# Performance work log

Hardware: AMD Instinct MI355X
Metric: run time of the kernel (lower is better)

## Reference

```python
import jax, jax.numpy as jnp
import numpy as np

B, T, D = 4, 2048, 256   # batch, temporal_scale, input_dim
H = 8                    # num_heads (hard-coded in module)
DH = D // H              # head dim
DFF = 512                # dim_feedforward (hard-coded)
WIN = 9                  # window_size
EPS = 1e-5               # LayerNorm eps


def _window_mask(t, h, w):
    # True = masked (disallowed). Each row j allows columns clip(j - w//2 + k, 0, t-1), k in [0, w).
    rows = jnp.arange(t)[:, None]                                   # [t,1]
    cols = jnp.clip(rows - w // 2 + jnp.arange(w)[None, :], 0, t - 1)  # [t,w]
    allowed = jnp.zeros((t, t), dtype=bool).at[rows, cols].set(True)
    # local_len == num_heads == 8: every head gets the same window mask
    return jnp.broadcast_to(~allowed, (h, t, t))                    # [H,T,T]


def setup_inputs() -> dict:
    key = jax.random.key(0)
    ks = jax.random.split(key, 6)
    s = 0.05
    return {
        "features": jax.random.normal(ks[0], (B, T, D), jnp.float32),
        "w_qkv": jax.random.normal(ks[1], (3 * D, D), jnp.float32) * s,
        "b_qkv": jnp.zeros((3 * D,), jnp.float32),
        "w_out": jax.random.normal(ks[2], (D, D), jnp.float32) * s,
        "b_out": jnp.zeros((D,), jnp.float32),
        "w1": jax.random.normal(ks[3], (DFF, D), jnp.float32) * s,
        "b1": jnp.zeros((DFF,), jnp.float32),
        "w2": jax.random.normal(ks[4], (D, DFF), jnp.float32) * s,
        "b2": jnp.zeros((D,), jnp.float32),
        "g1": jnp.ones((D,), jnp.float32),
        "be1": jnp.zeros((D,), jnp.float32),
        "g2": jnp.ones((D,), jnp.float32),
        "be2": jnp.zeros((D,), jnp.float32),
        "mask": _window_mask(T, H, WIN),
    }


def _layernorm(x, g, b):
    mu = jnp.mean(x, axis=-1, keepdims=True)
    var = jnp.var(x, axis=-1, keepdims=True)
    return (x - mu) * jax.lax.rsqrt(var + EPS) * g + b


def reference(features, w_qkv, b_qkv, w_out, b_out, w1, b1, w2, b2,
              g1, be1, g2, be2, mask):
    b, t, d = features.shape
    # --- windowed multi-head self-attention (dropout = eval-mode identity) ---
    qkv = features @ w_qkv.T + b_qkv                         # [b,t,3d]
    q, k, v = jnp.split(qkv, 3, axis=-1)
    split_heads = lambda x: x.reshape(b, t, H, DH).transpose(0, 2, 1, 3)  # [b,H,t,dh]
    q, k, v = split_heads(q), split_heads(k), split_heads(v)
    scores = jnp.einsum('bhqd,bhkd->bhqk', q, k) / jnp.sqrt(jnp.float32(DH))
    scores = jnp.where(mask[None], -jnp.inf, scores)         # mask True = disallowed
    attn = jax.nn.softmax(scores, axis=-1)                   # [b,H,t,t]
    o = jnp.einsum('bhqk,bhkd->bhqd', attn, v)
    o = o.transpose(0, 2, 1, 3).reshape(b, t, d)
    o = o @ w_out.T + b_out
    # --- residual + norm1 ---
    x = _layernorm(features + o, g1, be1)
    # --- FFN (relu) + residual + norm2 ---
    ff = jax.nn.relu(x @ w1.T + b1) @ w2.T + b2
    return _layernorm(x + ff, g2, be2)
```

## Files before the change

kernel.cpp:

```cpp
#include <hip/hip_runtime.h>
#include <math.h>

#define T_LEN 2048
#define LN_EPS 1e-5f
#define M_ROWS 8192

using u16x8  = __attribute__((ext_vector_type(8))) unsigned short;
using bf16x8 = __attribute__((ext_vector_type(8))) short;
using f32x4  = __attribute__((ext_vector_type(4))) float;

__device__ __forceinline__ unsigned short f2bf(float f) {
    unsigned int u = __float_as_uint(f);
    u += 0x7FFFu + ((u >> 16) & 1u);
    return (unsigned short)(u >> 16);
}
__device__ __forceinline__ float bf2f(unsigned short u) {
    return __uint_as_float(((unsigned int)u) << 16);
}
__device__ __forceinline__ u16x8 pack8(float4 a, float4 c) {
    u16x8 p;
    p[0] = f2bf(a.x); p[1] = f2bf(a.y); p[2] = f2bf(a.z); p[3] = f2bf(a.w);
    p[4] = f2bf(c.x); p[5] = f2bf(c.y); p[6] = f2bf(c.z); p[7] = f2bf(c.w);
    return p;
}
__device__ __forceinline__ void gload16(const void* g, void* l) {
    __builtin_amdgcn_global_load_lds(
        (const __attribute__((address_space(1))) unsigned int*)g,
        (__attribute__((address_space(3))) unsigned int*)l, 16, 0, 0);
}

__global__ __launch_bounds__(512) void qkv_gemm_f32(
    const float* __restrict__ A, const float* __restrict__ W,
    const float* __restrict__ bias,
    const float* __restrict__ wo, const float* __restrict__ w1,
    const float* __restrict__ w2,
    unsigned short* __restrict__ C, unsigned short* __restrict__ wconv)
{
    __shared__ char sm[2][40960];

    const int tid = threadIdx.x, lane = tid & 63, wid = tid >> 6;
    const int wr = wid >> 2, wcl = wid & 3;
    const int m0 = blockIdx.x * 128, n0 = blockIdx.y * 192;

    {
        const int bid = blockIdx.y * 64 + blockIdx.x;
        const int g = bid * 512 + tid;
        if (g < 40960) {
            const int e = g * 8;
            const float* src; int off;
            if (e < 65536)       { src = wo; off = 0; }
            else if (e < 196608) { src = w1; off = 65536; }
            else                 { src = w2; off = 196608; }
            const float4 a = *(const float4*)(src + (e - off));
            const float4 c = *(const float4*)(src + (e - off) + 4);
            *(u16x8*)(wconv + e) = pack8(a, c);
        }
    }

    float4 ld[5][2];
    auto LOADR = [&](int k0) {
        #pragma unroll
        for (int j = 0; j < 5; ++j) {
            const int i = j * 512 + tid;
            const float* src;
            if (i < 1024) {
                const int row = i >> 3, k8 = i & 7;
                src = A + (size_t)(m0 + row) * 256 + k0 + k8 * 8;
            } else {
                const int ii = i - 1024;
                const int row = ii >> 3, k8 = ii & 7;
                src = W + (size_t)(n0 + row) * 256 + k0 + k8 * 8;
            }
            ld[j][0] = *(const float4*)src;
            ld[j][1] = *(const float4*)(src + 4);
        }
    };
    auto CWRITE = [&](char* buf) {
        #pragma unroll
        for (int j = 0; j < 5; ++j) {
            const int i = j * 512 + tid;
            const u16x8 p = pack8(ld[j][0], ld[j][1]);
            if (i < 1024) {
                const int row = i >> 3, k8 = i & 7;
                *(u16x8*)(buf + ((row * 128 + k8 * 16) ^ ((row & 7) << 4))) = p;
            } else {
                const int ii = i - 1024;
                const int row = ii >> 3, k8 = ii & 7;
                *(u16x8*)(buf + 16384 + ((row * 128 + k8 * 16) ^ ((row & 7) << 4))) = p;
            }
        }
    };

    f32x4 acc[4][3];
    #pragma unroll
    for (int m = 0; m < 4; ++m)
        #pragma unroll
        for (int n = 0; n < 3; ++n) acc[m][n] = (f32x4)(0.f);

    LOADR(0);
    CWRITE(sm[0]);
    __syncthreads();

    #pragma unroll
    for (int k = 0; k < 4; ++k) {
        if (k < 3) LOADR((k + 1) * 64);
        char* As = sm[k & 1];
        char* Bs = sm[k & 1] + 16384;
        #pragma unroll
        for (int ks = 0; ks < 2; ++ks) {
            bf16x8 af[4], bfr[3];
            #pragma unroll
            for (int m = 0; m < 4; ++m) {
                const int row = wr * 64 + m * 16 + (lane & 15);
                const int off = (row * 128 + ks * 64 + (lane >> 4) * 16) ^ ((row & 7) << 4);
                af[m] = *(const bf16x8*)(As + off);
            }
            #pragma unroll
            for (int n = 0; n < 3; ++n) {
                const int row = wcl * 48 + n * 16 + (lane & 15);
                const int off = (row * 128 + ks * 64 + (lane >> 4) * 16) ^ ((row & 7) << 4);
                bfr[n] = *(const bf16x8*)(Bs + off);
            }
            #pragma unroll
            for (int m = 0; m < 4; ++m)
                #pragma unroll
                for (int n = 0; n < 3; ++n)
                    acc[m][n] = __builtin_amdgcn_mfma_f32_16x16x32_bf16(
                        af[m], bfr[n], acc[m][n], 0, 0, 0);
        }
        if (k < 3) CWRITE(sm[(k + 1) & 1]);
        __syncthreads();
    }

    #pragma unroll
    for (int n = 0; n < 3; ++n) {
        const int c = n0 + wcl * 48 + n * 16 + (lane & 15);
        const float bv = bias[c];
        #pragma unroll
        for (int m = 0; m < 4; ++m) {
            const int rbase = m0 + wr * 64 + m * 16 + ((lane >> 4) << 2);
            #pragma unroll
            for (int j = 0; j < 4; ++j)
                C[(size_t)(rbase + j) * 768 + c] = f2bf(acc[m][n][j] + bv);
        }
    }
}

__global__ __launch_bounds__(512) void tail_fused_db(
    const unsigned short* __restrict__ qkv, const unsigned short* __restrict__ Wo,
    const unsigned short* __restrict__ W1, const unsigned short* __restrict__ W2,
    const float* __restrict__ resf, const float* __restrict__ b_out,
    const float* __restrict__ g1, const float* __restrict__ be1,
    const float* __restrict__ b1, const float* __restrict__ b2,
    const float* __restrict__ g2, const float* __restrict__ be2,
    float* __restrict__ out)
{
    __shared__ __align__(16) char sm[116736];
    char* smA = sm;
    char* st[2] = { sm + 16384, sm + 49152 };
    char* smH = sm + 81920;
    float* part = (float*)(sm + 114688);

    const int tid = threadIdx.x, lane = tid & 63, wid = tid >> 6;
    const int m0 = blockIdx.x * 32;
    const int b = m0 >> 11, t0 = m0 & 2047;

    auto STAGE = [&](const unsigned short* W, int ldk, int rowoff, int k0, char* dst) {
        #pragma unroll
        for (int j = 0; j < 4; ++j) {
            const int i = j * 512 + tid, row = i >> 3, k8 = (i & 7) ^ (row & 7);
            gload16(W + (size_t)(rowoff + row) * ldk + k0 + k8 * 8, dst + i * 16);
        }
    };

    STAGE(Wo, 256, 0, 0, st[0]);
    {
        const int half = tid & 1, p = tid >> 1;
        const int h = p & 7, tl = p >> 3;
        const int t = t0 + tl;
        const unsigned short* base = qkv + (size_t)b * T_LEN * 768;

        float q[16];
        const unsigned short* qp = base + (size_t)t * 768 + h * 32 + half * 16;
        #pragma unroll
        for (int jj = 0; jj < 2; ++jj) {
            u16x8 u = *(const u16x8*)(qp + jj * 8);
            #pragma unroll
            for (int e = 0; e < 8; ++e) q[jj * 8 + e] = bf2f(u[e]);
        }
        const unsigned short* kbase = base + 256 + h * 32 + half * 16;
        const unsigned short* vbase = base + 512 + h * 32 + half * 16;

        float sc[9], mx = -1e30f;
        #pragma unroll
        for (int j = 0; j < 9; ++j) {
            const int kr0 = t - 4 + j;
            const int krm = min(max(kr0, 0), T_LEN - 1);
            const unsigned short* kr = kbase + (size_t)krm * 768;
            float d = 0.f;
            #pragma unroll
            for (int jj = 0; jj < 2; ++jj) {
                u16x8 u = *(const u16x8*)(kr + jj * 8);
                #pragma unroll
                for (int e = 0; e < 8; ++e) d += q[jj * 8 + e] * bf2f(u[e]);
            }
            d += __shfl_xor(d, 1);
            sc[j] = (kr0 == krm) ? d * 0.17677669529663687f : -1e30f;
            mx = fmaxf(mx, sc[j]);
        }
        float sum = 0.f;
        #pragma unroll
        for (int j = 0; j < 9; ++j) { sc[j] = expf(sc[j] - mx); sum += sc[j]; }
        const float inv = 1.f / sum;

        float ov[16] = {};
        #pragma unroll
        for (int j = 0; j < 9; ++j) {
            const float pj = sc[j] * inv;
            const int krm = min(max(t - 4 + j, 0), T_LEN - 1);
            const unsigned short* vr = vbase + (size_t)krm * 768;
            #pragma unroll
            for (int jj = 0; jj < 2; ++jj) {
                u16x8 u = *(const u16x8*)(vr + jj * 8);
                #pragma unroll
                for (int e = 0; e < 8; ++e) ov[jj * 8 + e] += pj * bf2f(u[e]);
            }
        }
        #pragma unroll
        for (int jj = 0; jj < 2; ++jj) {
            u16x8 p8;
            #pragma unroll
            for (int e = 0; e < 8; ++e) p8[e] = f2bf(ov[jj * 8 + e]);
            const int ch = h * 4 + half * 2 + jj;
            *(u16x8*)(smA + tl * 512 + ((ch ^ (tl & 7)) << 4)) = p8;
        }
    }
    __syncthreads();

    float xres[2][2][4];

    {
        f32x4 acc[2][2];
        #pragma unroll
        for (int m = 0; m < 2; ++m)
            #pragma unroll
            for (int n = 0; n < 2; ++n) acc[m][n] = (f32x4)(0.f);

        #pragma unroll
        for (int k = 0; k < 4; ++k) {
            if (k < 3) STAGE(Wo, 256, 0, (k + 1) * 64, st[(k + 1) & 1]);
            char* Bs = st[k & 1];
            #pragma unroll
            for (int ks = 0; ks < 2; ++ks) {
                bf16x8 af[2], bfr[2];
                #pragma unroll
                for (int m = 0; m < 2; ++m) {
                    const int r = m * 16 + (lane & 15);
                    const int ch = k * 8 + ks * 4 + (lane >> 4);
                    af[m] = *(const bf16x8*)(smA + r * 512 + ((ch ^ (r & 7)) << 4));
                }
                #pragma unroll
                for (int n = 0; n < 2; ++n) {
                    const int rB = wid * 32 + n * 16 + (lane & 15);
                    bfr[n] = *(const bf16x8*)(Bs + rB * 128
                             + (((ks * 4 + (lane >> 4)) ^ (rB & 7)) << 4));
                }
                #pragma unroll
                for (int m = 0; m < 2; ++m)
                    #pragma unroll
                    for (int n = 0; n < 2; ++n)
                        acc[m][n] = __builtin_amdgcn_mfma_f32_16x16x32_bf16(
                            af[m], bfr[n], acc[m][n], 0, 0, 0);
            }
            __syncthreads();
        }

        STAGE(W1, 256, 0, 0, st[0]);
        float v[2][2][4], s[2][4], sq[2][4];
        #pragma unroll
        for (int m = 0; m < 2; ++m)
            #pragma unroll
            for (int j = 0; j < 4; ++j) { s[m][j] = 0.f; sq[m][j] = 0.f; }
        #pragma unroll
        for (int n = 0; n < 2; ++n) {
            const int c = wid * 32 + n * 16 + (lane & 15);
            const float bv = b_out[c];
            #pragma unroll
            for (int m = 0; m < 2; ++m) {
                const int rb = m * 16 + ((lane >> 4) << 2);
                #pragma unroll
                for (int j = 0; j < 4; ++j) {
                    float x = acc[m][n][j] + bv + resf[(size_t)(m0 + rb + j) * 256 + c];
                    v[m][n][j] = x; s[m][j] += x; sq[m][j] += x * x;
                }
            }
        }
        #pragma unroll
        for (int m = 0; m < 2; ++m)
            #pragma unroll
            for (int j = 0; j < 4; ++j) {
                #pragma unroll
                for (int msk = 1; msk <= 8; msk <<= 1) {
                    s[m][j]  += __shfl_xor(s[m][j], msk);
                    sq[m][j] += __shfl_xor(sq[m][j], msk);
                }
                if ((lane & 15) == 0) {
                    const int r = m * 16 + ((lane >> 4) << 2) + j;
                    part[(wid * 32 + r) * 2 + 0] = s[m][j];
                    part[(wid * 32 + r) * 2 + 1] = sq[m][j];
                }
            }
        __syncthreads();
        #pragma unroll
        for (int m = 0; m < 2; ++m) {
            const int rb = m * 16 + ((lane >> 4) << 2);
            #pragma unroll
            for (int j = 0; j < 4; ++j) {
                const int r = rb + j;
                float S = 0.f, SQ = 0.f;
                #pragma unroll
                for (int w = 0; w < 8; ++w) {
                    S += part[(w * 32 + r) * 2 + 0]; SQ += part[(w * 32 + r) * 2 + 1];
                }
                const float mean = S * (1.f / 256.f);
                const float var  = SQ * (1.f / 256.f) - mean * mean;
                const float rstd = rsqrtf(var + LN_EPS);
                #pragma unroll
                for (int n = 0; n < 2; ++n) {
                    const int c = wid * 32 + n * 16 + (lane & 15);
                    const float o = (v[m][n][j] - mean) * rstd * g1[c] + be1[c];
                    xres[m][n][j] = o;
                    const int addr = r * 512 + (((c >> 3) ^ (r & 7)) << 4) + ((c & 7) << 1);
                    *(unsigned short*)(smA + addr) = f2bf(o);
                }
            }
        }
    }
    __syncthreads();

    {
        f32x4 acc[2][2];
        #pragma unroll
        for (int m = 0; m < 2; ++m)
            #pragma unroll
            for (int n = 0; n < 2; ++n) acc[m][n] = (f32x4)(0.f);

        #pragma unroll
        for (int r8 = 0; r8 < 8; ++r8) {
            const int half = r8 >> 2, kk = r8 & 3;
            if (r8 < 7) {
                const int nr = r8 + 1;
                STAGE(W1, 256, (nr >> 2) * 256, (nr & 3) * 64, st[nr & 1]);
            } else {
                STAGE(W2, 512, 0, 0, st[0]);
            }
            char* Bs = st[r8 & 1];
            #pragma unroll
            for (int ks = 0; ks < 2; ++ks) {
                bf16x8 af[2], bfr[2];
                #pragma unroll
                for (int m = 0; m < 2; ++m) {
                    const int r = m * 16 + (lane & 15);
                    const int ch = kk * 8 + ks * 4 + (lane >> 4);
                    af[m] = *(const bf16x8*)(smA + r * 512 + ((ch ^ (r & 7)) << 4));
                }
                #pragma unroll
                for (int n = 0; n < 2; ++n) {
                    const int rB = wid * 32 + n * 16 + (lane & 15);
                    bfr[n] = *(const bf16x8*)(Bs + rB * 128
                             + (((ks * 4 + (lane >> 4)) ^ (rB & 7)) << 4));
                }
                #pragma unroll
                for (int m = 0; m < 2; ++m)
                    #pragma unroll
                    for (int n = 0; n < 2; ++n)
                        acc[m][n] = __builtin_amdgcn_mfma_f32_16x16x32_bf16(
                            af[m], bfr[n], acc[m][n], 0, 0, 0);
            }
            __syncthreads();
            if (kk == 3) {
                #pragma unroll
                for (int n = 0; n < 2; ++n) {
                    const int c = half * 256 + wid * 32 + n * 16 + (lane & 15);
                    const float bv = b1[c];
                    #pragma unroll
                    for (int m = 0; m < 2; ++m) {
                        const int rb = m * 16 + ((lane >> 4) << 2);
                        #pragma unroll
                        for (int j = 0; j < 4; ++j) {
                            const int rr = rb + j;
                            const int addr = rr * 1024 + (((c >> 3) ^ (rr & 7)) << 4)
                                           + ((c & 7) << 1);
                            *(unsigned short*)(smH + addr) =
                                f2bf(fmaxf(acc[m][n][j] + bv, 0.f));
                        }
                    }
                }
                #pragma unroll
                for (int m = 0; m < 2; ++m)
                    #pragma unroll
                    for (int n = 0; n < 2; ++n) acc[m][n] = (f32x4)(0.f);
            }
        }
    }
    __syncthreads();

    {
        f32x4 acc[2][2];
        #pragma unroll
        for (int m = 0; m < 2; ++m)
            #pragma unroll
            for (int n = 0; n < 2; ++n) acc[m][n] = (f32x4)(0.f);

        #pragma unroll
        for (int k = 0; k < 8; ++k) {
            if (k < 7) STAGE(W2, 512, 0, (k + 1) * 64, st[(k + 1) & 1]);
            char* Bs = st[k & 1];
            #pragma unroll
            for (int ks = 0; ks < 2; ++ks) {
                bf16x8 af[2], bfr[2];
                #pragma unroll
                for (int m = 0; m < 2; ++m) {
                    const int r = m * 16 + (lane & 15);
                    const int ch = k * 8 + ks * 4 + (lane >> 4);
                    af[m] = *(const bf16x8*)(smH + r * 1024 + ((ch ^ (r & 7)) << 4));
                }
                #pragma unroll
                for (int n = 0; n < 2; ++n) {
                    const int rB = wid * 32 + n * 16 + (lane & 15);
                    bfr[n] = *(const bf16x8*)(Bs + rB * 128
                             + (((ks * 4 + (lane >> 4)) ^ (rB & 7)) << 4));
                }
                #pragma unroll
                for (int m = 0; m < 2; ++m)
                    #pragma unroll
                    for (int n = 0; n < 2; ++n)
                        acc[m][n] = __builtin_amdgcn_mfma_f32_16x16x32_bf16(
                            af[m], bfr[n], acc[m][n], 0, 0, 0);
            }
            __syncthreads();
        }

        float v[2][2][4], s[2][4], sq[2][4];
        #pragma unroll
        for (int m = 0; m < 2; ++m)
            #pragma unroll
            for (int j = 0; j < 4; ++j) { s[m][j] = 0.f; sq[m][j] = 0.f; }
        #pragma unroll
        for (int n = 0; n < 2; ++n) {
            const int c = wid * 32 + n * 16 + (lane & 15);
            const float bv = b2[c];
            #pragma unroll
            for (int m = 0; m < 2; ++m) {
                #pragma unroll
                for (int j = 0; j < 4; ++j) {
                    float x = acc[m][n][j] + bv + xres[m][n][j];
                    v[m][n][j] = x; s[m][j] += x; sq[m][j] += x * x;
                }
            }
        }
        #pragma unroll
        for (int m = 0; m < 2; ++m)
            #pragma unroll
            for (int j = 0; j < 4; ++j) {
                #pragma unroll
                for (int msk = 1; msk <= 8; msk <<= 1) {
                    s[m][j]  += __shfl_xor(s[m][j], msk);
                    sq[m][j] += __shfl_xor(sq[m][j], msk);
                }
                if ((lane & 15) == 0) {
                    const int r = m * 16 + ((lane >> 4) << 2) + j;
                    part[(wid * 32 + r) * 2 + 0] = s[m][j];
                    part[(wid * 32 + r) * 2 + 1] = sq[m][j];
                }
            }
        __syncthreads();
        #pragma unroll
        for (int m = 0; m < 2; ++m) {
            const int rb = m * 16 + ((lane >> 4) << 2);
            #pragma unroll
            for (int j = 0; j < 4; ++j) {
                const int r = rb + j;
                float S = 0.f, SQ = 0.f;
                #pragma unroll
                for (int w = 0; w < 8; ++w) {
                    S += part[(w * 32 + r) * 2 + 0]; SQ += part[(w * 32 + r) * 2 + 1];
                }
                const float mean = S * (1.f / 256.f);
                const float var  = SQ * (1.f / 256.f) - mean * mean;
                const float rstd = rsqrtf(var + LN_EPS);
                #pragma unroll
                for (int n = 0; n < 2; ++n) {
                    const int c = wid * 32 + n * 16 + (lane & 15);
                    out[(size_t)(m0 + r) * 256 + c] =
                        (v[m][n][j] - mean) * rstd * g2[c] + be2[c];
                }
            }
        }
    }
}

extern "C" void kernel_launch(void* const* d_in, const int* in_sizes, int n_in,
                              void* d_out, int out_size, void* d_ws, size_t ws_size,
                              hipStream_t stream) {
    const float* features = (const float*)d_in[0];
    const float* w_qkv    = (const float*)d_in[1];
    const float* b_qkv    = (const float*)d_in[2];
    const float* w_out    = (const float*)d_in[3];
    const float* b_out    = (const float*)d_in[4];
    const float* w1       = (const float*)d_in[5];
    const float* b1       = (const float*)d_in[6];
    const float* w2       = (const float*)d_in[7];
    const float* b2       = (const float*)d_in[8];
    const float* g1       = (const float*)d_in[9];
    const float* be1      = (const float*)d_in[10];
    const float* g2       = (const float*)d_in[11];
    const float* be2      = (const float*)d_in[12];

    unsigned short* wsu = (unsigned short*)d_ws;
    unsigned short* wconv = wsu;
    unsigned short* qkvbf = wsu + 327680;
    unsigned short* wobf  = wconv;
    unsigned short* w1bf  = wconv + 65536;
    unsigned short* w2bf  = wconv + 196608;

    qkv_gemm_f32<<<dim3(64, 4), 512, 0, stream>>>(
        features, w_qkv, b_qkv, w_out, w1, w2, qkvbf, wconv);
    tail_fused_db<<<M_ROWS / 32, 512, 0, stream>>>(
        qkvbf, wobf, w1bf, w2bf, features, b_out, g1, be1, b1, b2, g2, be2,
        (float*)d_out);
}
```

Baseline: 42.16 us.

## Triple-buffer weight staging with prefetch distance two across all tail GEMMs

Replaces the double-buffered per-GEMM weight staging with a single triple-buffered pipeline. It runs over all 20 weight tiles (Wo, W1, W2) and issues loads two tiles ahead, including across GEMM boundaries. Full __syncthreads barriers become s_waitcnt vmcnt(4) plus s_barrier, so the newest prefetch can stay in flight while the current tile is consumed. LDS use grows to about 146 KB, which should still allow one block per CU. The partial vmcnt wait relies on the order in which loads are counted.

```diff
diff --git a/kernel.cpp b/kernel.cpp
--- a/kernel.cpp
+++ b/kernel.cpp
@@ -27,6 +27,14 @@
     __builtin_amdgcn_global_load_lds(
         (const __attribute__((address_space(1))) unsigned int*)g,
         (__attribute__((address_space(3))) unsigned int*)l, 16, 0, 0);
+}
+__device__ __forceinline__ void bar_vm4() {
+    asm volatile("s_waitcnt vmcnt(4)" ::: "memory");
+    __builtin_amdgcn_s_barrier();
+}
+__device__ __forceinline__ void bar_vm0() {
+    asm volatile("s_waitcnt vmcnt(0)" ::: "memory");
+    __builtin_amdgcn_s_barrier();
 }
 
 __global__ __launch_bounds__(512) void qkv_gemm_f32(
@@ -146,7 +154,7 @@
     }
 }
 
-__global__ __launch_bounds__(512) void tail_fused_db(
+__global__ __launch_bounds__(512) void tail_fused_pipe(
     const unsigned short* __restrict__ qkv, const unsigned short* __restrict__ Wo,
     const unsigned short* __restrict__ W1, const unsigned short* __restrict__ W2,
     const float* __restrict__ resf, const float* __restrict__ b_out,
@@ -155,25 +163,32 @@
     const float* __restrict__ g2, const float* __restrict__ be2,
     float* __restrict__ out)
 {
-    __shared__ __align__(16) char sm[116736];
+    __shared__ __align__(16) char sm[149504];
     char* smA = sm;
-    char* st[2] = { sm + 16384, sm + 49152 };
-    char* smH = sm + 81920;
-    float* part = (float*)(sm + 114688);
+    char* smH = sm + 114688;
+    float* part = (float*)(sm + 147456);
 
     const int tid = threadIdx.x, lane = tid & 63, wid = tid >> 6;
     const int m0 = blockIdx.x * 32;
     const int b = m0 >> 11, t0 = m0 & 2047;
 
-    auto STAGE = [&](const unsigned short* W, int ldk, int rowoff, int k0, char* dst) {
+    auto stbuf = [&](int i) -> char* { return sm + 16384 + (i % 3) * 32768; };
+    auto NSTAGE = [&](int i) {
+        if (i >= 20) return;
+        const unsigned short* W; int ldk, ro, k0;
+        if (i < 4)       { W = Wo; ldk = 256; ro = 0;                    k0 = i * 64; }
+        else if (i < 12) { W = W1; ldk = 256; ro = ((i - 4) >> 2) * 256; k0 = ((i - 4) & 3) * 64; }
+        else             { W = W2; ldk = 512; ro = 0;                    k0 = (i - 12) * 64; }
+        char* dst = stbuf(i);
         #pragma unroll
         for (int j = 0; j < 4; ++j) {
-            const int i = j * 512 + tid, row = i >> 3, k8 = (i & 7) ^ (row & 7);
-            gload16(W + (size_t)(rowoff + row) * ldk + k0 + k8 * 8, dst + i * 16);
+            const int ii = j * 512 + tid, row = ii >> 3, k8 = (ii & 7) ^ (row & 7);
+            gload16(W + (size_t)(ro + row) * ldk + k0 + k8 * 8, dst + ii * 16);
         }
     };
 
-    STAGE(Wo, 256, 0, 0, st[0]);
+    NSTAGE(0); NSTAGE(1);
+
     {
         const int half = tid & 1, p = tid >> 1;
         const int h = p & 7, tl = p >> 3;
@@ -247,16 +262,16 @@
             for (int n = 0; n < 2; ++n) acc[m][n] = (f32x4)(0.f);
 
         #pragma unroll
-        for (int k = 0; k < 4; ++k) {
-            if (k < 3) STAGE(Wo, 256, 0, (k + 1) * 64, st[(k + 1) & 1]);
-            char* Bs = st[k & 1];
+        for (int i = 0; i < 4; ++i) {
+            NSTAGE(i + 2);
+            char* Bs = stbuf(i);
             #pragma unroll
             for (int ks = 0; ks < 2; ++ks) {
                 bf16x8 af[2], bfr[2];
                 #pragma unroll
                 for (int m = 0; m < 2; ++m) {
                     const int r = m * 16 + (lane & 15);
-                    const int ch = k * 8 + ks * 4 + (lane >> 4);
+                    const int ch = i * 8 + ks * 4 + (lane >> 4);
                     af[m] = *(const bf16x8*)(smA + r * 512 + ((ch ^ (r & 7)) << 4));
                 }
                 #pragma unroll
@@ -272,10 +287,9 @@
                         acc[m][n] = __builtin_amdgcn_mfma_f32_16x16x32_bf16(
                             af[m], bfr[n], acc[m][n], 0, 0, 0);
             }
-            __syncthreads();
-        }
-
-        STAGE(W1, 256, 0, 0, st[0]);
+            bar_vm4();
+        }
+
         float v[2][2][4], s[2][4], sq[2][4];
         #pragma unroll
         for (int m = 0; m < 2; ++m)
@@ -346,15 +360,10 @@
             for (int n = 0; n < 2; ++n) acc[m][n] = (f32x4)(0.f);
 
         #pragma unroll
-        for (int r8 = 0; r8 < 8; ++r8) {
-            const int half = r8 >> 2, kk = r8 & 3;
-            if (r8 < 7) {
-                const int nr = r8 + 1;
-                STAGE(W1, 256, (nr >> 2) * 256, (nr & 3) * 64, st[nr & 1]);
-            } else {
-                STAGE(W2, 512, 0, 0, st[0]);
-            }
-            char* Bs = st[r8 & 1];
+        for (int i = 4; i < 12; ++i) {
+            NSTAGE(i + 2);
+            const int kk = (i - 4) & 3, half = (i - 4) >> 2;
+            char* Bs = stbuf(i);
             #pragma unroll
             for (int ks = 0; ks < 2; ++ks) {
                 bf16x8 af[2], bfr[2];
@@ -377,7 +386,7 @@
                         acc[m][n] = __builtin_amdgcn_mfma_f32_16x16x32_bf16(
                             af[m], bfr[n], acc[m][n], 0, 0, 0);
             }
-            __syncthreads();
+            bar_vm4();
             if (kk == 3) {
                 #pragma unroll
                 for (int n = 0; n < 2; ++n) {
@@ -413,9 +422,10 @@
             for (int n = 0; n < 2; ++n) acc[m][n] = (f32x4)(0.f);
 
         #pragma unroll
-        for (int k = 0; k < 8; ++k) {
-            if (k < 7) STAGE(W2, 512, 0, (k + 1) * 64, st[(k + 1) & 1]);
-            char* Bs = st[k & 1];
+        for (int i = 12; i < 20; ++i) {
+            NSTAGE(i + 2);
+            const int k = i - 12;
+            char* Bs = stbuf(i);
             #pragma unroll
             for (int ks = 0; ks < 2; ++ks) {
                 bf16x8 af[2], bfr[2];
@@ -438,7 +448,7 @@
                         acc[m][n] = __builtin_amdgcn_mfma_f32_16x16x32_bf16(
                             af[m], bfr[n], acc[m][n], 0, 0, 0);
             }
-            __syncthreads();
+            if (i + 2 < 20) bar_vm4(); else bar_vm0();
         }
 
         float v[2][2][4], s[2][4], sq[2][4];
@@ -526,7 +536,7 @@
 
     qkv_gemm_f32<<<dim3(64, 4), 512, 0, stream>>>(
         features, w_qkv, b_qkv, w_out, w1, w2, qkvbf, wconv);
-    tail_fused_db<<<M_ROWS / 32, 512, 0, stream>>>(
+    tail_fused_pipe<<<M_ROWS / 32, 512, 0, stream>>>(
         qkvbf, wobf, w1bf, w2bf, features, b_out, g1, be1, b1, b2, g2, be2,
         (float*)d_out);
 }
```

After: 37.69 us. 1.12x faster.
